# Kernel optimization log

Hardware: AMD Instinct MI355X
Metric: run time of the kernel (lower is better)

The kernel has to match this reference:

```python
import jax, jax.numpy as jnp
import numpy as np

B, L, DM, DH = 8, 2048, 1024, 1024


def setup_inputs() -> dict:
    key = jax.random.key(0)
    ks = jax.random.split(key, 10)
    s_dm = 1.0 / np.sqrt(DM)   # nn.Linear(d_model, *) init bound
    s_dh = 1.0 / np.sqrt(DH)   # nn.Linear(d_hidden, *) init bound
    u = lambda k, shp, s: jax.random.uniform(k, shp, jnp.float32, -s, s)
    return {
        "x": jax.random.normal(ks[0], (B, L, DM), jnp.float32),
        # A scaled by 0.01 so cumprod(exp(delta*A)) stays finite over L=2048
        "A": 0.01 * jax.random.normal(ks[1], (DH,), jnp.float32),
        "Bw": u(ks[2], (DH, DM), s_dm), "Bb": u(ks[3], (DH,), s_dm),
        "Cw": u(ks[4], (DM, DH), s_dh), "Cb": u(ks[5], (DM,), s_dh),
        "Dw": u(ks[6], (DM, DM), s_dm), "Db": u(ks[7], (DM,), s_dm),
        "dw": u(ks[8], (DH, DM), s_dm), "db": u(ks[9], (DH,), s_dm),
    }


def reference(x, A, Bw, Bb, Cw, Cb, Dw, Db, dw, db):
    # x: [B, L, DM]
    delta = jax.nn.softplus(jnp.einsum('bld,hd->blh', x, dw) + db)   # [B,L,DH]
    A_bar = jnp.exp(delta * A)                                        # [B,L,DH]
    B_bar = delta * (jnp.einsum('bld,hd->blh', x, Bw) + Bb)           # [B,L,DH]
    A_cum = jnp.cumprod(A_bar, axis=1)                                # [B,L,DH]
    h = jnp.cumsum(B_bar / A_cum, axis=1) * A_cum                     # [B,L,DH]
    out = jnp.einsum('blh,dh->bld', h, Cw) + Cb \
        + jnp.einsum('bld,ed->ble', x, Dw) + Db                       # [B,L,DM]
    return out
```

## Files before the change

kernel.cpp:

```cpp
#include <hip/hip_runtime.h>
#include <hip/hip_bf16.h>
#include <stdint.h>

#define DMODEL 1024
#define DHID   1024
#define NBATCH 8
#define LSEQ   2048
#define MROWS  (NBATCH * LSEQ)
#define KCAT   2048
#define CH     32
#define NCH    64
#define BH     (NBATCH * DHID)
#define CPT    4

typedef __attribute__((ext_vector_type(8))) short  short8;
typedef __attribute__((ext_vector_type(4))) short  s16x4;
typedef __attribute__((ext_vector_type(8))) __bf16 bf16x8;
typedef __attribute__((ext_vector_type(4))) float  f32x4;

__device__ __forceinline__ unsigned short f2bf(float f) {
  union { float f; unsigned int u; } v; v.f = f;
  unsigned int u = v.u;
  u += 0x7fffu + ((u >> 16) & 1u);
  return (unsigned short)(u >> 16);
}

__device__ __forceinline__ float bf2f(unsigned short s) {
  union { unsigned int u; float f; } v; v.u = ((unsigned int)s) << 16;
  return v.f;
}

__device__ __forceinline__ float softplus_f(float x) {
  return fmaxf(x, 0.f) + log1pf(expf(-fabsf(x)));
}

__device__ __forceinline__ short8 pack8(float4 a, float4 b) {
  short8 o;
  o[0] = (short)f2bf(a.x); o[1] = (short)f2bf(a.y);
  o[2] = (short)f2bf(a.z); o[3] = (short)f2bf(a.w);
  o[4] = (short)f2bf(b.x); o[5] = (short)f2bf(b.y);
  o[6] = (short)f2bf(b.z); o[7] = (short)f2bf(b.w);
  return o;
}

__global__ __launch_bounds__(256)
void cast_all_kernel(const float* __restrict__ x,
                     const float* __restrict__ dw, const float* __restrict__ Bw,
                     const float* __restrict__ Cw, const float* __restrict__ Dw,
                     unsigned short* __restrict__ A2,
                     unsigned short* __restrict__ W1, unsigned short* __restrict__ W2) {
  const size_t MX = (size_t)MROWS * 1024;
  const size_t M1 = (size_t)1024 * 1024;
  size_t i8 = ((size_t)blockIdx.x * 256 + threadIdx.x) * 8;
  if (i8 < MX) {
    size_t row = i8 >> 10; int col = (int)(i8 & 1023);
    const float4* p = (const float4*)(x + i8);
    *(short8*)(A2 + row * (size_t)KCAT + 1024 + col) = pack8(p[0], p[1]);
  } else if (i8 < MX + 2 * M1) {
    size_t k = i8 - MX;
    const float* src = (k < M1) ? (dw + k) : (Bw + k - M1);
    const float4* p = (const float4*)src;
    *(short8*)(W1 + k) = pack8(p[0], p[1]);
  } else {
    size_t k = i8 - MX - 2 * M1;
    size_t d = k >> 11; int c = (int)(k & 2047);
    const float* src = (c < 1024) ? (Cw + d * 1024 + c) : (Dw + d * 1024 + (c - 1024));
    const float4* p = (const float4*)src;
    *(short8*)(W2 + k) = pack8(p[0], p[1]);
  }
}


__device__ __forceinline__ void stage_frag32(const unsigned short* __restrict__ gbase,
                                             int ld, int k0,
                                             unsigned short* sbase,
                                             int wave, int quad, int l16) {
#pragma unroll
  for (int s = 0; s < 2; ++s) {
    int f = s * 8 + wave;
    const unsigned short* g = gbase + (size_t)(f * 16 + l16) * ld + k0 + quad * 8;
    unsigned short* sd = sbase + (size_t)(s * 512 + wave * 64) * 8;
    __builtin_amdgcn_global_load_lds(
        (const __attribute__((address_space(1))) unsigned int*)g,
        (__attribute__((address_space(3))) unsigned int*)sd, 16, 0, 0);
  }
}

__global__ __launch_bounds__(512, 2)
void gemm256(const unsigned short* __restrict__ A, int lda,
             const unsigned short* __restrict__ B, int ldb,
             void* __restrict__ Cp, int ldc, int K, int mode,
             const float* __restrict__ bias0, const float* __restrict__ bias1) {
  __shared__ __align__(16) unsigned short smem[4 * 16384];
  const int tid  = threadIdx.x;
  const int lane = tid & 63;
  const int wave = tid >> 6;
  const int wr   = wave >> 2;
  const int wc   = wave & 3;
  const int quad = lane >> 4, l16 = lane & 15;

  const int Nt = gridDim.x, Mt = gridDim.y;
  int bid  = blockIdx.y * Nt + blockIdx.x;
  int xcd  = bid & 7;
  int slot = bid >> 3;
  int lm = slot / Nt;
  int ln = slot - lm * Nt;
  const int m0 = (xcd * (Mt >> 3) + lm) * 256;
  const int n0 = ln * 256;

  const unsigned short* Ab = A + (size_t)m0 * lda;
  const unsigned short* Bb = B + (size_t)n0 * ldb;

  const int nt = K >> 5;

  f32x4 acc[8][4] = {};

#pragma unroll
  for (int t = 0; t < 3; ++t) {
    unsigned short* buf = smem + t * 16384;
    stage_frag32(Ab, lda, t * 32, buf, wave, quad, l16);
    stage_frag32(Bb, ldb, t * 32, buf + 8192, wave, quad, l16);
  }
  asm volatile("s_waitcnt vmcnt(8)" ::: "memory");
  __builtin_amdgcn_s_barrier();
  __builtin_amdgcn_sched_barrier(0);

  for (int t = 0; t < nt; ++t) {
    const unsigned short* As = smem + (t & 3) * 16384;
    const unsigned short* Bs = As + 8192;
    unsigned short* nbuf = smem + ((t + 3) & 3) * 16384;
    const bool pf = (t + 3) < nt;
    const int kpf = (t + 3) * 32;
#pragma unroll
    for (int ph = 0; ph < 2; ++ph) {
      short8 af[4], bfr[4];
#pragma unroll
      for (int i = 0; i < 4; ++i)
        af[i] = *(const short8*)(As + (size_t)(wr * 8 + ph * 4 + i) * 512 + lane * 8);
#pragma unroll
      for (int j = 0; j < 4; ++j)
        bfr[j] = *(const short8*)(Bs + (size_t)(wc * 4 + j) * 512 + lane * 8);
      if (pf) {
        if (ph == 0) stage_frag32(Ab, lda, kpf, nbuf, wave, quad, l16);
        else         stage_frag32(Bb, ldb, kpf, nbuf + 8192, wave, quad, l16);
      }
      __builtin_amdgcn_s_barrier();
      __builtin_amdgcn_sched_barrier(0);
      __builtin_amdgcn_s_setprio(1);
#pragma unroll
      for (int i = 0; i < 4; ++i)
#pragma unroll
        for (int j = 0; j < 4; ++j)
          acc[ph * 4 + i][j] = __builtin_amdgcn_mfma_f32_16x16x32_bf16(
              __builtin_bit_cast(bf16x8, af[i]),
              __builtin_bit_cast(bf16x8, bfr[j]), acc[ph * 4 + i][j], 0, 0, 0);
      __builtin_amdgcn_s_setprio(0);
      if (ph == 1) {
        if (t + 3 < nt)      { asm volatile("s_waitcnt vmcnt(8)" ::: "memory"); }
        else if (t + 2 < nt) { asm volatile("s_waitcnt vmcnt(4)" ::: "memory"); }
        else if (t + 1 < nt) { asm volatile("s_waitcnt vmcnt(0)" ::: "memory"); }
      }
      __builtin_amdgcn_s_barrier();
      __builtin_amdgcn_sched_barrier(0);
    }
  }

  if (mode == 0) {
    float* C = (float*)Cp;
#pragma unroll
    for (int mi = 0; mi < 8; ++mi)
#pragma unroll
      for (int j = 0; j < 4; ++j) {
        int n  = n0 + wc * 64 + j * 16 + l16;
        int mb = m0 + wr * 128 + mi * 16 + quad * 4;
        float badd = bias0[n] + bias1[n];
#pragma unroll
        for (int r = 0; r < 4; ++r)
          C[(size_t)(mb + r) * ldc + n] = acc[mi][j][r] + badd;
      }
  } else {
    unsigned short* C16 = (unsigned short*)Cp;
#pragma unroll
    for (int mi = 0; mi < 8; ++mi)
#pragma unroll
      for (int j = 0; j < 4; ++j) {
        int n  = n0 + wc * 64 + j * 16 + l16;
        int mb = m0 + wr * 128 + mi * 16 + quad * 4;
#pragma unroll
        for (int r = 0; r < 4; ++r)
          C16[(size_t)(mb + r) * ldc + n] = f2bf(acc[mi][j][r]);
      }
  }
}

__global__ __launch_bounds__(256)
void scan_carry_kernel(unsigned short* __restrict__ G1,
                       const float* __restrict__ Av, const float* __restrict__ Bbv,
                       const float* __restrict__ dbv, float2* __restrict__ carr) {
  int t = blockIdx.x * 256 + threadIdx.x;
  int ho = t & 255, chunk = (t >> 8) & (NCH - 1), b = t >> 14;
  int h0 = ho << 2;
  float4 A0 = *(const float4*)(Av + h0);
  float4 B0 = *(const float4*)(Bbv + h0);
  float4 D0 = *(const float4*)(dbv + h0);
  float Ah[4]  = {A0.x, A0.y, A0.z, A0.w};
  float Bbh[4] = {B0.x, B0.y, B0.z, B0.w};
  float dbh[4] = {D0.x, D0.y, D0.z, D0.w};
  unsigned short* base = G1 + ((size_t)(b * LSEQ + chunk * CH)) * KCAT + h0;
  float hs[4] = {}, sd[4] = {};
  s16x4 dp = *(const s16x4*)(base);
  s16x4 bp = *(const s16x4*)(base + 1024);
#pragma unroll 4
  for (int l = 0; l < CH; ++l) {
    s16x4 dpn = dp, bpn = bp;
    if (l + 1 < CH) {
      dpn = *(const s16x4*)(base + (size_t)(l + 1) * KCAT);
      bpn = *(const s16x4*)(base + (size_t)(l + 1) * KCAT + 1024);
    }
    s16x4 dq, bq;
#pragma unroll
    for (int j = 0; j < 4; ++j) {
      float d = softplus_f(bf2f((unsigned short)dp[j]) + dbh[j]);
      unsigned short dr = f2bf(d);
      float drf = bf2f(dr);
      float bb = drf * (bf2f((unsigned short)bp[j]) + Bbh[j]);
      unsigned short br = f2bf(bb);
      sd[j] += drf;
      float a = __expf(drf * Ah[j]);
      hs[j] = fmaf(a, hs[j], bf2f(br));
      dq[j] = (short)dr; bq[j] = (short)br;
    }
    *(s16x4*)(base + (size_t)l * KCAT) = dq;
    *(s16x4*)(base + (size_t)l * KCAT + 1024) = bq;
    dp = dpn; bp = bpn;
  }
  float2* cb = carr + (size_t)chunk * BH + b * 1024 + h0;
#pragma unroll
  for (int j = 0; j < 4; ++j)
    cb[j] = make_float2(__expf(Ah[j] * sd[j]), hs[j]);
}

__global__ __launch_bounds__(256)
void scan_comb_kernel(const float2* __restrict__ carr, float* __restrict__ Hc) {
  int t = blockIdx.x * 256 + threadIdx.x;
  float H = 0.f;
#pragma unroll
  for (int c = 0; c < NCH; ++c) {
    float2 ah = carr[(size_t)c * BH + t];
    Hc[(size_t)c * BH + t] = H;
    H = fmaf(ah.x, H, ah.y);
  }
}

__global__ __launch_bounds__(256)
void scan_final_kernel(const unsigned short* __restrict__ G1,
                       const float* __restrict__ Av, const float* __restrict__ Hc,
                       unsigned short* __restrict__ A2) {
  int t = blockIdx.x * 256 + threadIdx.x;
  int ho = t & 255, chunk = (t >> 8) & (NCH - 1), b = t >> 14;
  int h0 = ho << 2;
  float4 A0 = *(const float4*)(Av + h0);
  float Ah[4] = {A0.x, A0.y, A0.z, A0.w};
  const unsigned short* base = G1 + ((size_t)(b * LSEQ + chunk * CH)) * KCAT + h0;
  unsigned short* obase = A2 + ((size_t)(b * LSEQ + chunk * CH)) * KCAT + h0;
  const float* hb = Hc + (size_t)chunk * BH + b * 1024 + h0;
  float hs[4];
#pragma unroll
  for (int j = 0; j < 4; ++j) hs[j] = hb[j];
  s16x4 dp = *(const s16x4*)(base);
  s16x4 bp = *(const s16x4*)(base + 1024);
#pragma unroll 4
  for (int l = 0; l < CH; ++l) {
    s16x4 dpn = dp, bpn = bp;
    if (l + 1 < CH) {
      dpn = *(const s16x4*)(base + (size_t)(l + 1) * KCAT);
      bpn = *(const s16x4*)(base + (size_t)(l + 1) * KCAT + 1024);
    }
    s16x4 o;
#pragma unroll
    for (int j = 0; j < 4; ++j) {
      float d = bf2f((unsigned short)dp[j]);
      float a = __expf(d * Ah[j]);
      hs[j] = fmaf(a, hs[j], bf2f((unsigned short)bp[j]));
      o[j] = (short)f2bf(hs[j]);
    }
    *(s16x4*)(obase + (size_t)l * KCAT) = o;
    dp = dpn; bp = bpn;
  }
}

extern "C" void kernel_launch(void* const* d_in, const int* in_sizes, int n_in,
                              void* d_out, int out_size, void* d_ws, size_t ws_size,
                              hipStream_t stream) {
  const float* x  = (const float*)d_in[0];
  const float* Av = (const float*)d_in[1];
  const float* Bw = (const float*)d_in[2];
  const float* Bb = (const float*)d_in[3];
  const float* Cw = (const float*)d_in[4];
  const float* Cb = (const float*)d_in[5];
  const float* Dw = (const float*)d_in[6];
  const float* Db = (const float*)d_in[7];
  const float* dw = (const float*)d_in[8];
  const float* db = (const float*)d_in[9];
  float* out = (float*)d_out;

  const size_t sz_big = (size_t)MROWS * KCAT * 2;
  const size_t sz_w   = (size_t)2048 * 1024 * 2;
  const size_t sz_hc  = (size_t)NCH * BH * 4;
  const size_t need = 2 * sz_big + 2 * sz_w + sz_hc;
  if (ws_size < need) return;

  char* w = (char*)d_ws;
  unsigned short* A2 = (unsigned short*)w; w += sz_big;
  unsigned short* G1 = (unsigned short*)w; w += sz_big;
  unsigned short* W1 = (unsigned short*)w; w += sz_w;
  unsigned short* W2 = (unsigned short*)w; w += sz_w;
  float* Hc = (float*)w;                   w += sz_hc;
  float2* carr = (float2*)W1;

  const size_t cast_elems = (size_t)MROWS * 1024 + 2 * (size_t)2048 * 1024;
  cast_all_kernel<<<(int)(cast_elems / (256 * 8)), 256, 0, stream>>>(
      x, dw, Bw, Cw, Dw, A2, W1, W2);

  dim3 g1(KCAT / 256, MROWS / 256);
  gemm256<<<g1, 512, 0, stream>>>(A2 + 1024, KCAT, W1, 1024, G1, KCAT, 1024, 1,
                                  nullptr, nullptr);

  scan_carry_kernel<<<(NBATCH * NCH * (DHID / CPT)) / 256, 256, 0, stream>>>(
      G1, Av, Bb, db, carr);
  scan_comb_kernel<<<BH / 256, 256, 0, stream>>>(carr, Hc);
  scan_final_kernel<<<(NBATCH * NCH * (DHID / CPT)) / 256, 256, 0, stream>>>(
      G1, Av, Hc, A2);

  dim3 g2(DMODEL / 256, MROWS / 256);
  gemm256<<<g2, 512, 0, stream>>>(A2, KCAT, W2, KCAT, out, DMODEL, KCAT, 0, Cb, Db);
}
```

Baseline: 372.1 us.

## Software-pipeline LDS fragment loads across K tiles in GEMM main loop

Restructures the GEMM main loop so the next tile's A and B fragments are read from LDS while the second half of the current tile's MFMAs is still pending. It double-buffers the B fragments in registers through an unroll-by-two macro and cuts the barriers per K tile from four to one. Both global prefetches are now issued at the start of each tile. This aims to hide LDS read latency and barrier stalls behind MFMA work, at the cost of more live registers under the 2-blocks-per-CU launch bound. It also assumes the number of K tiles is even.

```diff
diff --git a/kernel.cpp b/kernel.cpp
--- a/kernel.cpp
+++ b/kernel.cpp
@@ -86,6 +86,59 @@
   }
 }
 
+#define TILE_BODY(T, BCUR, BNXT)                                              \
+  {                                                                           \
+    const int t_ = (T);                                                       \
+    const unsigned short* As_ = smem + (t_ & 3) * 16384;                      \
+    if (t_ + 3 < nt) {                                                        \
+      unsigned short* nb_ = smem + ((t_ + 3) & 3) * 16384;                    \
+      stage_frag32(Ab, lda, (t_ + 3) * 32, nb_, wave, quad, l16);             \
+      stage_frag32(Bb, ldb, (t_ + 3) * 32, nb_ + 8192, wave, quad, l16);      \
+    }                                                                         \
+    _Pragma("unroll")                                                         \
+    for (int i = 0; i < 4; ++i)                                               \
+      af1[i] = *(const short8*)(As_ + (size_t)(wr * 8 + 4 + i) * 512 + lane * 8); \
+    __builtin_amdgcn_sched_barrier(0);                                        \
+    __builtin_amdgcn_s_setprio(1);                                            \
+    _Pragma("unroll")                                                         \
+    for (int i = 0; i < 4; ++i) {                                             \
+      _Pragma("unroll")                                                       \
+      for (int j = 0; j < 4; ++j)                                             \
+        acc[i][j] = __builtin_amdgcn_mfma_f32_16x16x32_bf16(                  \
+            __builtin_bit_cast(bf16x8, af0[i]),                               \
+            __builtin_bit_cast(bf16x8, BCUR[j]), acc[i][j], 0, 0, 0);         \
+    }                                                                         \
+    __builtin_amdgcn_s_setprio(0);                                            \
+    __builtin_amdgcn_sched_barrier(0);                                        \
+    asm volatile("s_waitcnt lgkmcnt(0)" ::: "memory");                        \
+    if (t_ + 3 < nt)      { asm volatile("s_waitcnt vmcnt(8)" ::: "memory"); }\
+    else if (t_ + 2 < nt) { asm volatile("s_waitcnt vmcnt(4)" ::: "memory"); }\
+    else if (t_ + 1 < nt) { asm volatile("s_waitcnt vmcnt(0)" ::: "memory"); }\
+    __builtin_amdgcn_s_barrier();                                             \
+    __builtin_amdgcn_sched_barrier(0);                                        \
+    if (t_ + 1 < nt) {                                                        \
+      const unsigned short* An_ = smem + ((t_ + 1) & 3) * 16384;              \
+      _Pragma("unroll")                                                       \
+      for (int j = 0; j < 4; ++j)                                             \
+        BNXT[j] = *(const short8*)(An_ + 8192 + (size_t)(wc * 4 + j) * 512 + lane * 8); \
+      _Pragma("unroll")                                                       \
+      for (int i = 0; i < 4; ++i)                                             \
+        af0[i] = *(const short8*)(An_ + (size_t)(wr * 8 + i) * 512 + lane * 8); \
+    }                                                                         \
+    __builtin_amdgcn_sched_barrier(0);                                        \
+    __builtin_amdgcn_s_setprio(1);                                            \
+    _Pragma("unroll")                                                         \
+    for (int i = 0; i < 4; ++i) {                                             \
+      _Pragma("unroll")                                                       \
+      for (int j = 0; j < 4; ++j)                                             \
+        acc[4 + i][j] = __builtin_amdgcn_mfma_f32_16x16x32_bf16(              \
+            __builtin_bit_cast(bf16x8, af1[i]),                               \
+            __builtin_bit_cast(bf16x8, BCUR[j]), acc[4 + i][j], 0, 0, 0);     \
+    }                                                                         \
+    __builtin_amdgcn_s_setprio(0);                                            \
+    __builtin_amdgcn_sched_barrier(0);                                        \
+  }
+
 __global__ __launch_bounds__(512, 2)
 void gemm256(const unsigned short* __restrict__ A, int lda,
              const unsigned short* __restrict__ B, int ldb,
@@ -114,6 +167,7 @@
   const int nt = K >> 5;
 
   f32x4 acc[8][4] = {};
+  short8 af0[4], af1[4], bfrE[4], bfrO[4];
 
 #pragma unroll
   for (int t = 0; t < 3; ++t) {
@@ -124,45 +178,17 @@
   asm volatile("s_waitcnt vmcnt(8)" ::: "memory");
   __builtin_amdgcn_s_barrier();
   __builtin_amdgcn_sched_barrier(0);
-
-  for (int t = 0; t < nt; ++t) {
-    const unsigned short* As = smem + (t & 3) * 16384;
-    const unsigned short* Bs = As + 8192;
-    unsigned short* nbuf = smem + ((t + 3) & 3) * 16384;
-    const bool pf = (t + 3) < nt;
-    const int kpf = (t + 3) * 32;
-#pragma unroll
-    for (int ph = 0; ph < 2; ++ph) {
-      short8 af[4], bfr[4];
-#pragma unroll
-      for (int i = 0; i < 4; ++i)
-        af[i] = *(const short8*)(As + (size_t)(wr * 8 + ph * 4 + i) * 512 + lane * 8);
-#pragma unroll
-      for (int j = 0; j < 4; ++j)
-        bfr[j] = *(const short8*)(Bs + (size_t)(wc * 4 + j) * 512 + lane * 8);
-      if (pf) {
-        if (ph == 0) stage_frag32(Ab, lda, kpf, nbuf, wave, quad, l16);
-        else         stage_frag32(Bb, ldb, kpf, nbuf + 8192, wave, quad, l16);
-      }
-      __builtin_amdgcn_s_barrier();
-      __builtin_amdgcn_sched_barrier(0);
-      __builtin_amdgcn_s_setprio(1);
-#pragma unroll
-      for (int i = 0; i < 4; ++i)
-#pragma unroll
-        for (int j = 0; j < 4; ++j)
-          acc[ph * 4 + i][j] = __builtin_amdgcn_mfma_f32_16x16x32_bf16(
-              __builtin_bit_cast(bf16x8, af[i]),
-              __builtin_bit_cast(bf16x8, bfr[j]), acc[ph * 4 + i][j], 0, 0, 0);
-      __builtin_amdgcn_s_setprio(0);
-      if (ph == 1) {
-        if (t + 3 < nt)      { asm volatile("s_waitcnt vmcnt(8)" ::: "memory"); }
-        else if (t + 2 < nt) { asm volatile("s_waitcnt vmcnt(4)" ::: "memory"); }
-        else if (t + 1 < nt) { asm volatile("s_waitcnt vmcnt(0)" ::: "memory"); }
-      }
-      __builtin_amdgcn_s_barrier();
-      __builtin_amdgcn_sched_barrier(0);
-    }
+#pragma unroll
+  for (int j = 0; j < 4; ++j)
+    bfrE[j] = *(const short8*)(smem + 8192 + (size_t)(wc * 4 + j) * 512 + lane * 8);
+#pragma unroll
+  for (int i = 0; i < 4; ++i)
+    af0[i] = *(const short8*)(smem + (size_t)(wr * 8 + i) * 512 + lane * 8);
+  __builtin_amdgcn_sched_barrier(0);
+
+  for (int t = 0; t < nt; t += 2) {
+    TILE_BODY(t,     bfrE, bfrO)
+    TILE_BODY(t + 1, bfrO, bfrE)
   }
 
   if (mode == 0) {
```

Measured after the change: 371.5 us. About the same (-0.2%).
